# Performance work log

Measured on AMD Instinct MI355X. Metric: run time of the kernel, lower is better.

The kernel has to match this reference:

```python
import jax, jax.numpy as jnp
import numpy as np

N_EMBD = 1024
N_HEAD = 16


def setup_inputs() -> dict:
    key = jax.random.key(0)
    k1, k2, k3, k4, k5 = jax.random.split(key, 5)
    B, T, C = 4, 2048, N_EMBD
    s = 1.0 / np.sqrt(C)
    x = jax.random.normal(k1, (B, T, C), dtype=jnp.float32)
    w_weight = jax.random.normal(k2, (3 * C, C), dtype=jnp.float32) * s
    w_bias = jax.random.normal(k3, (3 * C,), dtype=jnp.float32) * s
    proj_weight = jax.random.normal(k4, (C, C), dtype=jnp.float32) * s
    proj_bias = jax.random.normal(k5, (C,), dtype=jnp.float32) * s
    return {"x": x, "w_weight": w_weight, "w_bias": w_bias,
            "proj_weight": proj_weight, "proj_bias": proj_bias}


def reference(x, w_weight, w_bias, proj_weight, proj_bias):
    B, T, C = x.shape
    nh = N_HEAD
    hs = C // nh
    # fused QKV projection (torch Linear: x @ W^T + b)
    wei = jnp.einsum('btc,oc->bto', x, w_weight) + w_bias
    k, q, v = jnp.split(wei, 3, axis=-1)  # note: chunk order is k, q, v
    # [B, T, nh, hs] -> [B, nh, T, hs]
    key_ = k.reshape(B, T, nh, hs).transpose(0, 2, 1, 3)
    query = q.reshape(B, T, nh, hs).transpose(0, 2, 1, 3)
    value = v.reshape(B, T, nh, hs).transpose(0, 2, 1, 3)
    scale = hs ** (-0.5)
    weight = jnp.einsum('bhqd,bhkd->bhqk', query, key_) * scale
    weight = jax.nn.softmax(weight, axis=-1)
    out = jnp.einsum('bhqk,bhkd->bhqd', weight, value)  # [B, nh, T, hs]
    # Faithful to source bug: transpose(1,2) is discarded; view is taken on
    # the (B, nh, T, hs) layout directly.
    out = out.reshape(B, T, C)
    out = jnp.einsum('btc,oc->bto', out, proj_weight) + proj_bias
    return out
```

## Files before the change

kernel.cpp:

```cpp
#include <hip/hip_runtime.h>
#include <hip/hip_bf16.h>


typedef __attribute__((ext_vector_type(8)))  short bf16x8;
typedef __attribute__((ext_vector_type(4)))  float f32x4;
typedef __attribute__((ext_vector_type(16))) float f32x16;
typedef __attribute__((ext_vector_type(2)))  unsigned u32x2;

typedef __attribute__((address_space(3))) unsigned lds_u32_t;
typedef __attribute__((address_space(1))) unsigned glb_u32_t;

__device__ __forceinline__ void async_cp16(const short* g, short* l) {
    __builtin_amdgcn_global_load_lds((glb_u32_t*)g, (lds_u32_t*)l, 16, 0, 0);
}

__device__ __forceinline__ float exp2fast(float x) {
    return __builtin_amdgcn_exp2f(x);
}

__device__ __forceinline__ short f2bf(float f) {
    union { float f; unsigned u; } v; v.f = f;
    unsigned r = v.u + 0x7fffu + ((v.u >> 16) & 1u);
    return (short)(r >> 16);
}

__device__ __forceinline__ unsigned cvt_pk_bf16(float lo, float hi) {
    unsigned r;
    asm("v_cvt_pk_bf16_f32 %0, %1, %2" : "=v"(r) : "v"(lo), "v"(hi));
    return r;
}

__global__ __launch_bounds__(256) void cvt3_kernel(
    const float4* __restrict__ x,  const float4* __restrict__ ww,
    const float4* __restrict__ pw, short4* __restrict__ xb,
    short4* __restrict__ wwb,      short4* __restrict__ pwb) {
    const int b = blockIdx.x;
    const float4* in; short4* out; int i;
    if (b < 8192)       { in = x;  out = xb;  i = b * 256 + threadIdx.x; }
    else if (b < 11264) { in = ww; out = wwb; i = (b - 8192) * 256 + threadIdx.x; }
    else                { in = pw; out = pwb; i = (b - 11264) * 256 + threadIdx.x; }
    float4 v = in[i];
    short4 o;
    o.x = f2bf(v.x); o.y = f2bf(v.y); o.z = f2bf(v.z); o.w = f2bf(v.w);
    out[i] = o;
}

template<int EPI>
__global__ __launch_bounds__(256) void gemm_bf16(
    const short* __restrict__ A, const short* __restrict__ W,
    const float* __restrict__ bias, float* __restrict__ outF,
    short* __restrict__ kout, short* __restrict__ qout, short* __restrict__ vtout,
    int M, int N, int K)
{
    __shared__ short lA[2][128 * 64];
    __shared__ short lB[2][128 * 64];
    const int tid  = threadIdx.x;
    const int lane = tid & 63;
    const int wave = tid >> 6;
    const int wM = (wave >> 1) * 64;
    const int wN = (wave & 1) * 64;
    const int l15 = lane & 15, l4 = lane >> 4;
    const int rsw = (lane & 7) << 3;

    const int lin = blockIdx.y * gridDim.x + blockIdx.x;
    const int byp = 8 * (lin & 7) + ((lin >> 3) & 7);
    const int bxp = lin >> 6;
    const int rowBase = byp * 128;
    const int colBase = bxp * 128;

    auto STAGE = [&](int t, int buf) {
        const int k0 = t * 64;
        #pragma unroll
        for (int i = 0; i < 4; ++i) {
            int idx = i * 256 + tid;
            int r   = idx >> 3;
            int cp  = ((idx & 7) ^ (r & 7)) * 8;
            int eo  = idx * 8;
            async_cp16(A + (size_t)(rowBase + r) * K + k0 + cp, &lA[buf][eo]);
            async_cp16(W + (size_t)(colBase + r) * K + k0 + cp, &lB[buf][eo]);
        }
    };

    f32x4 acc[4][4] = {};
    const int NT = K >> 6;

    STAGE(0, 0);
    __syncthreads();

    int cur = 0;
    for (int t = 0; t < NT; ++t) {
        if (t + 1 < NT) STAGE(t + 1, cur ^ 1);
        #pragma unroll
        for (int kt = 0; kt < 2; ++kt) {
            bf16x8 af[4], bfr[4];
            #pragma unroll
            for (int mt = 0; mt < 4; ++mt)
                af[mt] = *(const bf16x8*)(
                    &lA[cur][(wM + mt * 16 + l15) * 64 + ((kt * 32 + l4 * 8) ^ rsw)]);
            #pragma unroll
            for (int nt = 0; nt < 4; ++nt)
                bfr[nt] = *(const bf16x8*)(
                    &lB[cur][(wN + nt * 16 + l15) * 64 + ((kt * 32 + l4 * 8) ^ rsw)]);
            #pragma unroll
            for (int mt = 0; mt < 4; ++mt)
                #pragma unroll
                for (int nt = 0; nt < 4; ++nt)
                    acc[mt][nt] = __builtin_amdgcn_mfma_f32_16x16x32_bf16(
                        af[mt], bfr[nt], acc[mt][nt], 0, 0, 0);
        }
        __syncthreads();
        cur ^= 1;
    }

    #pragma unroll
    for (int mt = 0; mt < 4; ++mt) {
        #pragma unroll
        for (int nt = 0; nt < 4; ++nt) {
            const int n  = colBase + wN + nt * 16 + l15;
            const int mb = rowBase + wM + mt * 16 + l4 * 4;
            const float bv = bias[n];
            #pragma unroll
            for (int r = 0; r < 4; ++r) {
                const int m = mb + r;
                float val = acc[mt][nt][r] + bv;
                if (EPI == 0) {
                    int b = m >> 11, t = m & 2047;
                    int j = n >> 10, hd = n & 1023;
                    int h = hd >> 6, d = hd & 63;
                    size_t base = ((size_t)(b * 16 + h) * 2048 + t) * 64 + d;
                    if (j == 0)      kout[base] = f2bf(val);
                    else if (j == 1) qout[base] = f2bf(val * 0.180336879f);
                    else             vtout[((size_t)(b * 16 + h) * 64 + d) * 2048 + t] = f2bf(val);
                } else {
                    outF[(size_t)m * N + n] = val;
                }
            }
        }
    }
}

__global__ __launch_bounds__(256) void attn_kernel(
    const short* __restrict__ Q, const short* __restrict__ Km,
    const short* __restrict__ Vt, short* __restrict__ O)
{
    __shared__ short kbuf[2][64 * 64];
    __shared__ short vbuf[2][64 * 64];

    const int tid  = threadIdx.x;
    const int lane = tid & 63;
    const int wave = tid >> 6;
    const int l31 = lane & 31;
    const int l1  = lane >> 5;

    const int b     = blockIdx.x;
    const int xcd   = b & 7;
    const int inner = b >> 3;
    const int bx    = inner & 15;
    const int bh    = xcd * 8 + (inner >> 4);
    const int q0    = bx * 128 + wave * 32;

    const short* Qh = Q  + (size_t)bh * 2048 * 64;
    const short* Kh = Km + (size_t)bh * 2048 * 64;
    const short* Vh = Vt + (size_t)bh * 64 * 2048;

    const int i8 = lane >> 3, i7 = lane & 7;
    const int srcCol = 8 * (i7 ^ i8);
    const int rsw    = (l31 & 7) << 3;

    const short* src[4];
    short* dst0[4];
    int step;
    if (wave < 2) {
        #pragma unroll
        for (int c = 0; c < 4; ++c) {
            int j = wave * 4 + c;
            src[c]  = Kh + (size_t)(8 * j + i8) * 64 + srcCol;
            dst0[c] = &kbuf[0][j * 512 + lane * 8];
        }
        step = 64 * 64;
    } else {
        #pragma unroll
        for (int c = 0; c < 4; ++c) {
            int j = (wave - 2) * 4 + c;
            src[c]  = Vh + (size_t)(8 * j + i8) * 2048 + srcCol;
            dst0[c] = &vbuf[0][j * 512 + lane * 8];
        }
        step = 64;
    }
    auto STAGE = [&](int buf) {
        #pragma unroll
        for (int c = 0; c < 4; ++c) {
            async_cp16(src[c], dst0[c] + buf * 4096);
            src[c] += step;
        }
    };

    bf16x8 qf[4];
    #pragma unroll
    for (int s = 0; s < 4; ++s)
        qf[s] = *(const bf16x8*)(Qh + (size_t)(q0 + l31) * 64 + s * 16 + l1 * 8);

    union { unsigned u[4]; bf16x8 v; } onesu;
    #pragma unroll
    for (int j = 0; j < 4; ++j) onesu.u[j] = 0x3F803F80u;
    const bf16x8 onesf = onesu.v;

    f32x16 o[2] = {};
    f32x16 ol   = {};

    STAGE(0);
    __syncthreads();

    int cur = 0;
    for (int it = 0; it < 32; ++it) {
        if (it < 31) STAGE(cur ^ 1);

        f32x16 s2[2] = {};
        __builtin_amdgcn_s_setprio(1);
        #pragma unroll
        for (int t = 0; t < 2; ++t) {
            #pragma unroll
            for (int s = 0; s < 4; ++s) {
                bf16x8 kf = *(const bf16x8*)(
                    &kbuf[cur][(t * 32 + l31) * 64 + ((s * 16 + l1 * 8) ^ rsw)]);
                s2[t] = __builtin_amdgcn_mfma_f32_32x32x16_bf16(kf, qf[s], s2[t], 0, 0, 0);
            }
        }
        __builtin_amdgcn_s_setprio(0);

        #pragma unroll
        for (int t = 0; t < 2; ++t)
            #pragma unroll
            for (int i = 0; i < 16; ++i)
                s2[t][i] = exp2fast(s2[t][i]);

        bf16x8 pa[4];
        #pragma unroll
        for (int t = 0; t < 2; ++t) {
            #pragma unroll
            for (int sl = 0; sl < 2; ++sl) {
                unsigned A0 = cvt_pk_bf16(s2[t][8 * sl + 0], s2[t][8 * sl + 1]);
                unsigned A1 = cvt_pk_bf16(s2[t][8 * sl + 2], s2[t][8 * sl + 3]);
                unsigned B0 = cvt_pk_bf16(s2[t][8 * sl + 4], s2[t][8 * sl + 5]);
                unsigned B1 = cvt_pk_bf16(s2[t][8 * sl + 6], s2[t][8 * sl + 7]);
                u32x2 ra = __builtin_amdgcn_permlane32_swap(A0, B0, false, false);
                u32x2 rb = __builtin_amdgcn_permlane32_swap(A1, B1, false, false);
                union { unsigned u[4]; bf16x8 v; } w;
                w.u[0] = ra.x;
                w.u[1] = rb.x;
                w.u[2] = ra.y;
                w.u[3] = rb.y;
                pa[2 * t + sl] = w.v;
            }
        }

        __builtin_amdgcn_s_setprio(1);
        #pragma unroll
        for (int s = 0; s < 4; ++s) {
            #pragma unroll
            for (int dt = 0; dt < 2; ++dt) {
                bf16x8 vf = *(const bf16x8*)(
                    &vbuf[cur][(dt * 32 + l31) * 64 + ((s * 16 + l1 * 8) ^ rsw)]);
                o[dt] = __builtin_amdgcn_mfma_f32_32x32x16_bf16(pa[s], vf, o[dt], 0, 0, 0);
            }
            ol = __builtin_amdgcn_mfma_f32_32x32x16_bf16(pa[s], onesf, ol, 0, 0, 0);
        }
        __builtin_amdgcn_s_setprio(0);

        __syncthreads();
        cur ^= 1;
    }

    #pragma unroll
    for (int g = 0; g < 4; ++g)
        #pragma unroll
        for (int rr = 0; rr < 4; ++rr) {
            float invl = 1.f / ol[g * 4 + rr];
            int qrow = q0 + rr + 8 * g + 4 * l1;
            size_t base = ((size_t)bh * 2048 + qrow) * 64 + l31;
            O[base]      = f2bf(o[0][g * 4 + rr] * invl);
            O[base + 32] = f2bf(o[1][g * 4 + rr] * invl);
        }
}

extern "C" void kernel_launch(void* const* d_in, const int* in_sizes, int n_in,
                              void* d_out, int out_size, void* d_ws, size_t ws_size,
                              hipStream_t stream) {
    const float* x  = (const float*)d_in[0];
    const float* ww = (const float*)d_in[1];
    const float* wb = (const float*)d_in[2];
    const float* pwt = (const float*)d_in[3];
    const float* pb  = (const float*)d_in[4];
    float* out = (float*)d_out;

    short* ws  = (short*)d_ws;
    short* xb  = ws;
    short* wwb = xb  + 8192 * 1024;
    short* pwb = wwb + 3072 * 1024;
    short* qb  = pwb + 1024 * 1024;
    short* kb  = qb  + 64 * 2048 * 64;
    short* vtb = kb  + 64 * 2048 * 64;
    short* ob  = vtb + 64 * 2048 * 64;

    cvt3_kernel<<<12288, 256, 0, stream>>>(
        (const float4*)x, (const float4*)ww, (const float4*)pwt,
        (short4*)xb, (short4*)wwb, (short4*)pwb);

    gemm_bf16<0><<<dim3(24, 64), 256, 0, stream>>>(
        xb, wwb, wb, nullptr, kb, qb, vtb, 8192, 3072, 1024);

    attn_kernel<<<1024, 256, 0, stream>>>(qb, kb, vtb, ob);

    gemm_bf16<1><<<dim3(8, 64), 256, 0, stream>>>(
        ob, pwb, pb, out, nullptr, nullptr, nullptr, 8192, 1024, 1024);
}
```

Baseline: 205.4 us.

## Software-pipeline attention loop: overlap next QK^T with current softmax-PV

New measurement: 198.7 us, median of 2. -3.2%, faster.

```diff
diff --git a/kernel.cpp b/kernel.cpp
--- a/kernel.cpp
+++ b/kernel.cpp
@@ -187,11 +187,22 @@
         }
         step = 64;
     }
-    auto STAGE = [&](int buf) {
-        #pragma unroll
-        for (int c = 0; c < 4; ++c) {
-            async_cp16(src[c], dst0[c] + buf * 4096);
-            src[c] += step;
+    auto STAGE_K = [&](int buf) {
+        if (wave < 2) {
+            #pragma unroll
+            for (int c = 0; c < 4; ++c) {
+                async_cp16(src[c], dst0[c] + buf * 4096);
+                src[c] += step;
+            }
+        }
+    };
+    auto STAGE_V = [&](int buf) {
+        if (wave >= 2) {
+            #pragma unroll
+            for (int c = 0; c < 4; ++c) {
+                async_cp16(src[c], dst0[c] + buf * 4096);
+                src[c] += step;
+            }
         }
     };
 
@@ -207,33 +218,30 @@
 
     f32x16 o[2] = {};
     f32x16 ol   = {};
-
-    STAGE(0);
-    __syncthreads();
-
-    int cur = 0;
-    for (int it = 0; it < 32; ++it) {
-        if (it < 31) STAGE(cur ^ 1);
-
-        f32x16 s2[2] = {};
+    f32x16 s2a[2], s2b[2];
+
+    auto QK = [&](int kb, f32x16* out) {
+        f32x16 r0 = {}, r1 = {};
         __builtin_amdgcn_s_setprio(1);
         #pragma unroll
-        for (int t = 0; t < 2; ++t) {
-            #pragma unroll
-            for (int s = 0; s < 4; ++s) {
-                bf16x8 kf = *(const bf16x8*)(
-                    &kbuf[cur][(t * 32 + l31) * 64 + ((s * 16 + l1 * 8) ^ rsw)]);
-                s2[t] = __builtin_amdgcn_mfma_f32_32x32x16_bf16(kf, qf[s], s2[t], 0, 0, 0);
-            }
+        for (int s = 0; s < 4; ++s) {
+            bf16x8 kf0 = *(const bf16x8*)(
+                &kbuf[kb][(l31) * 64 + ((s * 16 + l1 * 8) ^ rsw)]);
+            r0 = __builtin_amdgcn_mfma_f32_32x32x16_bf16(kf0, qf[s], r0, 0, 0, 0);
+            bf16x8 kf1 = *(const bf16x8*)(
+                &kbuf[kb][(32 + l31) * 64 + ((s * 16 + l1 * 8) ^ rsw)]);
+            r1 = __builtin_amdgcn_mfma_f32_32x32x16_bf16(kf1, qf[s], r1, 0, 0, 0);
         }
         __builtin_amdgcn_s_setprio(0);
-
+        out[0] = r0; out[1] = r1;
+    };
+
+    auto SMPV = [&](f32x16* s2, int vb) {
         #pragma unroll
         for (int t = 0; t < 2; ++t)
             #pragma unroll
             for (int i = 0; i < 16; ++i)
                 s2[t][i] = exp2fast(s2[t][i]);
-
         bf16x8 pa[4];
         #pragma unroll
         for (int t = 0; t < 2; ++t) {
@@ -253,23 +261,43 @@
                 pa[2 * t + sl] = w.v;
             }
         }
-
         __builtin_amdgcn_s_setprio(1);
         #pragma unroll
         for (int s = 0; s < 4; ++s) {
             #pragma unroll
             for (int dt = 0; dt < 2; ++dt) {
                 bf16x8 vf = *(const bf16x8*)(
-                    &vbuf[cur][(dt * 32 + l31) * 64 + ((s * 16 + l1 * 8) ^ rsw)]);
+                    &vbuf[vb][(dt * 32 + l31) * 64 + ((s * 16 + l1 * 8) ^ rsw)]);
                 o[dt] = __builtin_amdgcn_mfma_f32_32x32x16_bf16(pa[s], vf, o[dt], 0, 0, 0);
             }
             ol = __builtin_amdgcn_mfma_f32_32x32x16_bf16(pa[s], onesf, ol, 0, 0, 0);
         }
         __builtin_amdgcn_s_setprio(0);
-
+    };
+
+    STAGE_K(0);
+    __syncthreads();
+    STAGE_K(1);
+    STAGE_V(0);
+    QK(0, s2a);
+    __syncthreads();
+    for (int i = 0; i < 15; ++i) {
+        STAGE_K(0);
+        STAGE_V(1);
+        QK(1, s2b);
+        SMPV(s2a, 0);
         __syncthreads();
-        cur ^= 1;
+        STAGE_K(1);
+        STAGE_V(0);
+        QK(0, s2a);
+        SMPV(s2b, 1);
+        __syncthreads();
     }
+    STAGE_V(1);
+    QK(1, s2b);
+    SMPV(s2a, 0);
+    __syncthreads();
+    SMPV(s2b, 1);
 
     #pragma unroll
     for (int g = 0; g < 4; ++g)
```
